# Kernel optimization log

Hardware: AMD Instinct MI355X
Metric: run time of the kernel (lower is better)

## Reference

```python
import jax, jax.numpy as jnp
import numpy as np

N, T, V = 32, 4096, 3
H = 512
CONNECTIVITY = 0.3
SPECTRAL_RADIUS = 0.99
NOISE_LEVEL = 0.01
N_DROP = 0


def _init_internal_weights(h, connectivity, spectral_radius):
    # Mirrors sparse.rand(...).todense(); nonzeros shifted by -0.5; normalized
    # so max |eigenvalue| == spectral_radius.
    rng = np.random.default_rng(0)
    w = rng.random((h, h)).astype(np.float32)
    mask = rng.random((h, h)) < connectivity
    w = np.where(mask, w - 0.5, 0.0).astype(np.float32)
    e_max = np.abs(np.linalg.eigvals(w)).max()
    w = w / (e_max / spectral_radius)
    return jnp.asarray(w, dtype=jnp.float32)


def setup_inputs() -> dict:
    key = jax.random.key(0)
    k_x, k_in, k_noise = jax.random.split(key, 3)
    X = jax.random.normal(k_x, (N, T, V), dtype=jnp.float32)
    # input weights: (2*bernoulli(U(0,1)) - 1) * 0.2  -> random signs * 0.2
    signs = 2.0 * jax.random.bernoulli(k_in, 0.5, (H, V)).astype(jnp.float32) - 1.0
    W_in = signs * 0.2
    W_int = _init_internal_weights(H, CONNECTIVITY, SPECTRAL_RADIUS)
    # per-step uniform noise, pre-drawn: (T, N, H)
    noise = jax.random.uniform(k_noise, (T, N, H), dtype=jnp.float32)
    return {"X": X, "W_in": W_in, "W_int": W_int, "noise": noise}


def reference(X, W_in, W_int, noise):
    # X: (N, T, V); W_in: (H, V); W_int: (H, H); noise: (T, N, H)
    n, t, _ = X.shape
    h = W_int.shape[0]
    # einsum('bij,kj->bki', X, W_in) indexed [:, :, t] == per-step input (N, H)
    inputs = jnp.einsum('btv,hv->tbh', X, W_in)  # (T, N, H)
    prev0 = jnp.full((n, h), 0.01, dtype=X.dtype)

    def step(prev, xs):
        x_t, n_t = xs
        s = jnp.tanh(prev @ W_int + x_t + n_t * NOISE_LEVEL)
        return s, s

    _, states = jax.lax.scan(step, prev0, (inputs, noise))  # (T, N, H)
    states = jnp.transpose(states, (1, 0, 2))  # (N, T, H)
    return states[:, N_DROP:, :]
```

## Files before the change

### kernel.cpp

```cpp
#include <hip/hip_runtime.h>
#include <stdint.h>

typedef _Float16 h2 __attribute__((ext_vector_type(2)));
typedef float    f4 __attribute__((ext_vector_type(4)));
typedef uint32_t u4 __attribute__((ext_vector_type(4)));

#if __has_builtin(__builtin_amdgcn_fdot2)
__device__ __forceinline__ float dot2(uint32_t a, uint32_t b, float c) {
    return __builtin_amdgcn_fdot2(__builtin_bit_cast(h2, a),
                                  __builtin_bit_cast(h2, b), c, false);
}
#else
__device__ __forceinline__ float dot2(uint32_t a, uint32_t b, float c) {
    h2 ha = __builtin_bit_cast(h2, a), hb = __builtin_bit_cast(h2, b);
    return c + (float)ha[0]*(float)hb[0] + (float)ha[1]*(float)hb[1];
}
#endif

__device__ __forceinline__ float fast_tanh(float z) {
    float e = __expf(2.0f * z);
    return 1.0f - 2.0f * __builtin_amdgcn_rcpf(e + 1.0f);
}

#define TT 4096
#define NB 32
#define HD 512
#define JL 12
#define JTOT 64
#define JR (JTOT - JL)

__global__ __launch_bounds__(512, 1)
void esn_kernel(const float* __restrict__ X, const float* __restrict__ W_in,
                const float* __restrict__ W_int, const float* __restrict__ noise,
                float* __restrict__ out)
{
    __shared__ __align__(16) _Float16 s_buf[2][HD];
    __shared__ float pads[4][HD];
    __shared__ u4 wstash[8 * JL * 64];

    const int tid  = threadIdx.x;
    const int b    = blockIdx.x;
    const int w    = tid >> 6;
    const int l    = tid & 63;
    const int kg   = tid >> 7;
    const int colg = tid & 127;
    const int c0   = colg * 4;

    const float win0 = W_in[tid*3 + 0];
    const float win1 = W_in[tid*3 + 1];
    const float win2 = W_in[tid*3 + 2];

    uint32_t wreg[4][JR];
    {
        const f4* Wv = (const f4*)W_int;
        for (int j = 0; j < JL; ++j) {
            const int k = kg*128 + 2*j;
            f4 r0 = Wv[(size_t)k*128 + colg];
            f4 r1 = Wv[(size_t)(k+1)*128 + colg];
            u4 q;
            #pragma unroll
            for (int c = 0; c < 4; ++c) {
                h2 hw; hw[0] = (_Float16)r0[c]; hw[1] = (_Float16)r1[c];
                q[c] = __builtin_bit_cast(uint32_t, hw);
            }
            wstash[(w*JL + j)*64 + l] = q;
        }
        #pragma unroll
        for (int j = 0; j < JR; ++j) {
            const int k = kg*128 + 2*(JL + j);
            f4 r0 = Wv[(size_t)k*128 + colg];
            f4 r1 = Wv[(size_t)(k+1)*128 + colg];
            #pragma unroll
            for (int c = 0; c < 4; ++c) {
                h2 hw; hw[0] = (_Float16)r0[c]; hw[1] = (_Float16)r1[c];
                wreg[c][j] = __builtin_bit_cast(uint32_t, hw);
            }
        }
    }
    s_buf[0][tid] = (_Float16)0.01f;
    __syncthreads();

    const float* Xb   = X   + (size_t)b * TT * 3;
    float*       outb = out + (size_t)b * TT * HD;
    const size_t nb   = (size_t)b * HD + tid;

    int cur = 0;
    for (int t = 0; t < TT; ++t) {
        const float nz = noise[(size_t)t*(NB*HD) + nb];
        const float x0 = Xb[t*3 + 0];
        const float x1 = Xb[t*3 + 1];
        const float x2 = Xb[t*3 + 2];

        const u4* sv4 = (const u4*)((const uint32_t*)(&s_buf[cur][0]) + kg*64);
        float a0 = 0.f, a1 = 0.f, a2 = 0.f, a3 = 0.f;
        u4 sq;

        #pragma unroll
        for (int j = 0; j < JL; ++j) {
            if ((j & 3) == 0) sq = sv4[j >> 2];
            const uint32_t sv = sq[j & 3];
            u4 q = wstash[(w*JL + j)*64 + l];
            a0 = dot2(sv, q[0], a0);
            a1 = dot2(sv, q[1], a1);
            a2 = dot2(sv, q[2], a2);
            a3 = dot2(sv, q[3], a3);
        }
        #pragma unroll
        for (int j = 0; j < JR; ++j) {
            const int jg = JL + j;
            if ((jg & 3) == 0) sq = sv4[jg >> 2];
            const uint32_t sv = sq[jg & 3];
            a0 = dot2(sv, wreg[0][j], a0);
            a1 = dot2(sv, wreg[1][j], a1);
            a2 = dot2(sv, wreg[2][j], a2);
            a3 = dot2(sv, wreg[3][j], a3);
        }
        f4 pv; pv[0] = a0; pv[1] = a1; pv[2] = a2; pv[3] = a3;
        *(f4*)&pads[kg][c0] = pv;
        __syncthreads();

        float z = pads[0][tid] + pads[1][tid] + pads[2][tid] + pads[3][tid];
        z += win0*x0 + win1*x1 + win2*x2 + 0.01f*nz;
        const float s = fast_tanh(z);
        outb[(size_t)t*HD + tid] = s;
        s_buf[cur^1][tid] = (_Float16)s;
        __syncthreads();
        cur ^= 1;
    }
}

extern "C" void kernel_launch(void* const* d_in, const int* in_sizes, int n_in,
                              void* d_out, int out_size, void* d_ws, size_t ws_size,
                              hipStream_t stream)
{
    const float* X     = (const float*)d_in[0];
    const float* W_in  = (const float*)d_in[1];
    const float* W_int = (const float*)d_in[2];
    const float* noise = (const float*)d_in[3];
    float* out = (float*)d_out;

    esn_kernel<<<dim3(NB), dim3(512), 0, stream>>>(X, W_in, W_int, noise, out);
}
```

Measured before the change: 5.376 ms.

## Split each batch row across two cooperating blocks with flag-based state exchange

```diff
diff --git a/kernel.cpp b/kernel.cpp
--- a/kernel.cpp
+++ b/kernel.cpp
@@ -5,17 +5,10 @@
 typedef float    f4 __attribute__((ext_vector_type(4)));
 typedef uint32_t u4 __attribute__((ext_vector_type(4)));
 
-#if __has_builtin(__builtin_amdgcn_fdot2)
 __device__ __forceinline__ float dot2(uint32_t a, uint32_t b, float c) {
     return __builtin_amdgcn_fdot2(__builtin_bit_cast(h2, a),
                                   __builtin_bit_cast(h2, b), c, false);
 }
-#else
-__device__ __forceinline__ float dot2(uint32_t a, uint32_t b, float c) {
-    h2 ha = __builtin_bit_cast(h2, a), hb = __builtin_bit_cast(h2, b);
-    return c + (float)ha[0]*(float)hb[0] + (float)ha[1]*(float)hb[1];
-}
-#endif
 
 __device__ __forceinline__ float fast_tanh(float z) {
     float e = __expf(2.0f * z);
@@ -23,14 +16,140 @@
 }
 
 #define TT 4096
-#define NB 32
+#define NBAT 32
 #define HD 512
+#define HALF 256
+#define FSTRIDE 4100
+#define FLAGS_BYTES (64 * FSTRIDE * 4)
+#define PUB_OFF 1114112
+#define WS_NEED (PUB_OFF + (size_t)64 * 2 * HALF * 2)
+
+#define DOTQ(sq, q)                                                          \
+    if ((q) & 1) {                                                           \
+        d0b = dot2((sq)[0], wr0[4*(q)+0], d0b);                              \
+        d0b = dot2((sq)[1], wr0[4*(q)+1], d0b);                              \
+        d0b = dot2((sq)[2], wr0[4*(q)+2], d0b);                              \
+        d0b = dot2((sq)[3], wr0[4*(q)+3], d0b);                              \
+        d1b = dot2((sq)[0], wr1[4*(q)+0], d1b);                              \
+        d1b = dot2((sq)[1], wr1[4*(q)+1], d1b);                              \
+        d1b = dot2((sq)[2], wr1[4*(q)+2], d1b);                              \
+        d1b = dot2((sq)[3], wr1[4*(q)+3], d1b);                              \
+    } else {                                                                 \
+        d0a = dot2((sq)[0], wr0[4*(q)+0], d0a);                              \
+        d0a = dot2((sq)[1], wr0[4*(q)+1], d0a);                              \
+        d0a = dot2((sq)[2], wr0[4*(q)+2], d0a);                              \
+        d0a = dot2((sq)[3], wr0[4*(q)+3], d0a);                              \
+        d1a = dot2((sq)[0], wr1[4*(q)+0], d1a);                              \
+        d1a = dot2((sq)[1], wr1[4*(q)+1], d1a);                              \
+        d1a = dot2((sq)[2], wr1[4*(q)+2], d1a);                              \
+        d1a = dot2((sq)[3], wr1[4*(q)+3], d1a);                              \
+    }
+
+__global__ __launch_bounds__(512, 1)
+void esn_pair(const float* __restrict__ X, const float* __restrict__ W_in,
+              const float* __restrict__ W_int, const float* __restrict__ noise,
+              float* __restrict__ out, int* flags, _Float16* pub)
+{
+    __shared__ __align__(16) _Float16 s_buf[2][HALF];
+    __shared__ float pads[4][HALF];
+
+    const int tid  = threadIdx.x;
+    const int bid  = blockIdx.x;
+    const int row  = (bid >> 4) * 8 + (bid & 7);
+    const int side = (bid >> 3) & 1;
+    const int hb   = side * HALF;
+    const int pr   = bid ^ 8;
+    const int kh   = tid >> 7;
+    const int colg = tid & 127;
+    const int c0   = hb + colg * 2;
+
+    const int ksb = ((kh < 2) ? hb : (hb ^ HALF)) + (kh & 1) * 128;
+
+    uint32_t wr0[64], wr1[64];
+    #pragma unroll
+    for (int p = 0; p < 64; ++p) {
+        const int k = ksb + 2 * p;
+        h2 a, b;
+        a[0] = (_Float16)W_int[(size_t)k * HD + c0];
+        a[1] = (_Float16)W_int[(size_t)(k + 1) * HD + c0];
+        b[0] = (_Float16)W_int[(size_t)k * HD + c0 + 1];
+        b[1] = (_Float16)W_int[(size_t)(k + 1) * HD + c0 + 1];
+        wr0[p] = __builtin_bit_cast(uint32_t, a);
+        wr1[p] = __builtin_bit_cast(uint32_t, b);
+    }
+    float win0 = 0.f, win1 = 0.f, win2 = 0.f;
+    if (tid < HALF) {
+        const int mc = hb + tid;
+        win0 = W_in[mc*3 + 0]; win1 = W_in[mc*3 + 1]; win2 = W_in[mc*3 + 2];
+        s_buf[0][tid] = (_Float16)0.01f;
+    }
+    __syncthreads();
+
+    const float* Xb     = X   + (size_t)row * TT * 3;
+    float*       outb   = out + (size_t)row * TT * HD;
+    int*         myflag = flags + bid * FSTRIDE;
+    const int*   prflag = flags + pr  * FSTRIDE;
+    _Float16*       mypub = pub + (size_t)bid * 2 * HALF;
+    const _Float16* prpub = pub + (size_t)pr  * 2 * HALF;
+
+    int cur = 0;
+    for (int t = 0; t < TT; ++t) {
+        float nz = 0.f, x0 = 0.f, x1 = 0.f, x2 = 0.f;
+        if (tid < HALF) {
+            nz = noise[((size_t)t * NBAT + row) * HD + hb + tid];
+            x0 = Xb[t*3 + 0]; x1 = Xb[t*3 + 1]; x2 = Xb[t*3 + 2];
+        }
+
+        float d0a = 0.f, d0b = 0.f, d1a = 0.f, d1b = 0.f;
+        if (kh < 2) {
+            const u4* sb4 = ((const u4*)&s_buf[cur][0]) + (kh & 1) * 16;
+            #pragma unroll
+            for (int q = 0; q < 16; ++q) { const u4 sq = sb4[q]; DOTQ(sq, q); }
+        } else if (t > 0) {
+            const int* fp = prflag + t;
+            int guard = 0;
+            while (__hip_atomic_load(fp, __ATOMIC_ACQUIRE,
+                                     __HIP_MEMORY_SCOPE_AGENT) == 0) {
+                __builtin_amdgcn_s_sleep(1);
+                if (++guard > 65536) break;
+            }
+            const u4* pb4 = ((const u4*)(prpub + (size_t)(t & 1) * HALF))
+                            + (kh & 1) * 16;
+            asm volatile("" : "+v"(pb4));
+            #pragma unroll
+            for (int q = 0; q < 16; ++q) { const u4 sq = pb4[q]; DOTQ(sq, q); }
+        } else {
+            h2 cc; cc[0] = (_Float16)0.01f; cc[1] = (_Float16)0.01f;
+            const uint32_t c01 = __builtin_bit_cast(uint32_t, cc);
+            u4 sq; sq[0] = c01; sq[1] = c01; sq[2] = c01; sq[3] = c01;
+            #pragma unroll
+            for (int q = 0; q < 16; ++q) { DOTQ(sq, q); }
+        }
+        *(float2*)&pads[kh][colg * 2] = make_float2(d0a + d0b, d1a + d1b);
+        __syncthreads();
+
+        if (tid < HALF) {
+            float z = pads[0][tid] + pads[1][tid] + pads[2][tid] + pads[3][tid]
+                    + win0*x0 + win1*x1 + win2*x2 + 0.01f*nz;
+            const float s = fast_tanh(z);
+            outb[(size_t)t * HD + hb + tid] = s;
+            s_buf[cur ^ 1][tid] = (_Float16)s;
+            mypub[(size_t)((t + 1) & 1) * HALF + tid] = (_Float16)s;
+        }
+        __syncthreads();
+        if (tid == 0)
+            __hip_atomic_store(myflag + (t + 1), 1, __ATOMIC_RELEASE,
+                               __HIP_MEMORY_SCOPE_AGENT);
+        cur ^= 1;
+    }
+}
+
 #define JL 12
 #define JTOT 64
 #define JR (JTOT - JL)
 
 __global__ __launch_bounds__(512, 1)
-void esn_kernel(const float* __restrict__ X, const float* __restrict__ W_in,
+void esn_single(const float* __restrict__ X, const float* __restrict__ W_in,
                 const float* __restrict__ W_int, const float* __restrict__ noise,
                 float* __restrict__ out)
 {
@@ -86,7 +205,7 @@
 
     int cur = 0;
     for (int t = 0; t < TT; ++t) {
-        const float nz = noise[(size_t)t*(NB*HD) + nb];
+        const float nz = noise[(size_t)t*(NBAT*HD) + nb];
         const float x0 = Xb[t*3 + 0];
         const float x1 = Xb[t*3 + 1];
         const float x2 = Xb[t*3 + 2];
@@ -139,5 +258,12 @@
     const float* noise = (const float*)d_in[3];
     float* out = (float*)d_out;
 
-    esn_kernel<<<dim3(NB), dim3(512), 0, stream>>>(X, W_in, W_int, noise, out);
-}
+    if (ws_size >= WS_NEED) {
+        hipMemsetAsync(d_ws, 0, FLAGS_BYTES, stream);
+        esn_pair<<<dim3(64), dim3(512), 0, stream>>>(
+            X, W_in, W_int, noise, out,
+            (int*)d_ws, (_Float16*)((char*)d_ws + PUB_OFF));
+    } else {
+        esn_single<<<dim3(32), dim3(512), 0, stream>>>(X, W_in, W_int, noise, out);
+    }
+}
```

Result: slower. 20.03 ms (+272.6%).

## Interleave LDS-stashed weight rows with register rows and software-pipeline LDS loads

Applied to the files above, without the earlier changes.

```diff
diff --git a/kernel.cpp b/kernel.cpp
--- a/kernel.cpp
+++ b/kernel.cpp
@@ -5,17 +5,10 @@
 typedef float    f4 __attribute__((ext_vector_type(4)));
 typedef uint32_t u4 __attribute__((ext_vector_type(4)));
 
-#if __has_builtin(__builtin_amdgcn_fdot2)
 __device__ __forceinline__ float dot2(uint32_t a, uint32_t b, float c) {
     return __builtin_amdgcn_fdot2(__builtin_bit_cast(h2, a),
                                   __builtin_bit_cast(h2, b), c, false);
 }
-#else
-__device__ __forceinline__ float dot2(uint32_t a, uint32_t b, float c) {
-    h2 ha = __builtin_bit_cast(h2, a), hb = __builtin_bit_cast(h2, b);
-    return c + (float)ha[0]*(float)hb[0] + (float)ha[1]*(float)hb[1];
-}
-#endif
 
 __device__ __forceinline__ float fast_tanh(float z) {
     float e = __expf(2.0f * z);
@@ -25,9 +18,8 @@
 #define TT 4096
 #define NB 32
 #define HD 512
-#define JL 12
-#define JTOT 64
-#define JR (JTOT - JL)
+#define NLQ 12
+#define NRJ 52
 
 __global__ __launch_bounds__(512, 1)
 void esn_kernel(const float* __restrict__ X, const float* __restrict__ W_in,
@@ -36,7 +28,8 @@
 {
     __shared__ __align__(16) _Float16 s_buf[2][HD];
     __shared__ float pads[4][HD];
-    __shared__ u4 wstash[8 * JL * 64];
+    __shared__ u4 wstash[8 * NLQ * 64];
+    __shared__ float win_lds[HD][3];
 
     const int tid  = threadIdx.x;
     const int b    = blockIdx.x;
@@ -46,14 +39,15 @@
     const int colg = tid & 127;
     const int c0   = colg * 4;
 
-    const float win0 = W_in[tid*3 + 0];
-    const float win1 = W_in[tid*3 + 1];
-    const float win2 = W_in[tid*3 + 2];
+    win_lds[tid][0] = W_in[tid*3 + 0];
+    win_lds[tid][1] = W_in[tid*3 + 1];
+    win_lds[tid][2] = W_in[tid*3 + 2];
 
-    uint32_t wreg[4][JR];
+    uint32_t wreg[4][NRJ];
     {
         const f4* Wv = (const f4*)W_int;
-        for (int j = 0; j < JL; ++j) {
+        #pragma unroll
+        for (int j = 0; j < 64; ++j) {
             const int k = kg*128 + 2*j;
             f4 r0 = Wv[(size_t)k*128 + colg];
             f4 r1 = Wv[(size_t)(k+1)*128 + colg];
@@ -63,17 +57,12 @@
                 h2 hw; hw[0] = (_Float16)r0[c]; hw[1] = (_Float16)r1[c];
                 q[c] = __builtin_bit_cast(uint32_t, hw);
             }
-            wstash[(w*JL + j)*64 + l] = q;
-        }
-        #pragma unroll
-        for (int j = 0; j < JR; ++j) {
-            const int k = kg*128 + 2*(JL + j);
-            f4 r0 = Wv[(size_t)k*128 + colg];
-            f4 r1 = Wv[(size_t)(k+1)*128 + colg];
-            #pragma unroll
-            for (int c = 0; c < 4; ++c) {
-                h2 hw; hw[0] = (_Float16)r0[c]; hw[1] = (_Float16)r1[c];
-                wreg[c][j] = __builtin_bit_cast(uint32_t, hw);
+            if (j % 5 == 0 && j < 56) {
+                wstash[(w*NLQ + j/5)*64 + l] = q;
+            } else {
+                const int ri = j - (j < 56 ? j/5 + 1 : 12);
+                wreg[0][ri] = q[0]; wreg[1][ri] = q[1];
+                wreg[2][ri] = q[2]; wreg[3][ri] = q[3];
             }
         }
     }
@@ -83,50 +72,58 @@
     const float* Xb   = X   + (size_t)b * TT * 3;
     float*       outb = out + (size_t)b * TT * HD;
     const size_t nb   = (size_t)b * HD + tid;
+    const u4*    wv   = &wstash[(w*NLQ)*64 + l];
 
+    float o_prev = 0.f;
     int cur = 0;
     for (int t = 0; t < TT; ++t) {
+        if (t > 0) outb[(size_t)(t-1)*HD + tid] = o_prev;
         const float nz = noise[(size_t)t*(NB*HD) + nb];
         const float x0 = Xb[t*3 + 0];
         const float x1 = Xb[t*3 + 1];
         const float x2 = Xb[t*3 + 2];
 
         const u4* sv4 = (const u4*)((const uint32_t*)(&s_buf[cur][0]) + kg*64);
+        u4 sqs[3] = {sv4[0], sv4[1], sv4[2]};
+        u4 wl[2]  = {wv[0], wv[64]};
         float a0 = 0.f, a1 = 0.f, a2 = 0.f, a3 = 0.f;
-        u4 sq;
 
         #pragma unroll
-        for (int j = 0; j < JL; ++j) {
-            if ((j & 3) == 0) sq = sv4[j >> 2];
-            const uint32_t sv = sq[j & 3];
-            u4 q = wstash[(w*JL + j)*64 + l];
-            a0 = dot2(sv, q[0], a0);
-            a1 = dot2(sv, q[1], a1);
-            a2 = dot2(sv, q[2], a2);
-            a3 = dot2(sv, q[3], a3);
-        }
-        #pragma unroll
-        for (int j = 0; j < JR; ++j) {
-            const int jg = JL + j;
-            if ((jg & 3) == 0) sq = sv4[jg >> 2];
-            const uint32_t sv = sq[jg & 3];
-            a0 = dot2(sv, wreg[0][j], a0);
-            a1 = dot2(sv, wreg[1][j], a1);
-            a2 = dot2(sv, wreg[2][j], a2);
-            a3 = dot2(sv, wreg[3][j], a3);
+        for (int j = 0; j < 64; ++j) {
+            const int g = j >> 2;
+            if ((j & 3) == 0 && g >= 1 && g <= 13)
+                sqs[(g - 1) % 3] = sv4[g + 2];
+            const uint32_t sv = sqs[g % 3][j & 3];
+            if (j % 5 == 0 && j < 56) {
+                const int i = j / 5;
+                const u4 q = wl[i & 1];
+                a0 = dot2(sv, q[0], a0);
+                a1 = dot2(sv, q[1], a1);
+                a2 = dot2(sv, q[2], a2);
+                a3 = dot2(sv, q[3], a3);
+                if (i + 2 < NLQ) wl[i & 1] = wv[(i + 2) * 64];
+            } else {
+                const int ri = j - (j < 56 ? j/5 + 1 : 12);
+                a0 = dot2(sv, wreg[0][ri], a0);
+                a1 = dot2(sv, wreg[1][ri], a1);
+                a2 = dot2(sv, wreg[2][ri], a2);
+                a3 = dot2(sv, wreg[3][ri], a3);
+            }
         }
         f4 pv; pv[0] = a0; pv[1] = a1; pv[2] = a2; pv[3] = a3;
         *(f4*)&pads[kg][c0] = pv;
         __syncthreads();
 
         float z = pads[0][tid] + pads[1][tid] + pads[2][tid] + pads[3][tid];
-        z += win0*x0 + win1*x1 + win2*x2 + 0.01f*nz;
+        z += win_lds[tid][0]*x0 + win_lds[tid][1]*x1 + win_lds[tid][2]*x2
+           + 0.01f*nz;
         const float s = fast_tanh(z);
-        outb[(size_t)t*HD + tid] = s;
+        o_prev = s;
         s_buf[cur^1][tid] = (_Float16)s;
         __syncthreads();
         cur ^= 1;
     }
+    outb[(size_t)(TT-1)*HD + tid] = o_prev;
 }
 
 extern "C" void kernel_launch(void* const* d_in, const int* in_sizes, int n_in,
```

Measured after the change: 5.696 ms. 6.0% more time.
